# Kernel tuning notes

Hardware: AMD Instinct MI355X
Metric: run time of the kernel (lower is better)

The kernel has to match this reference:

```python
import jax, jax.numpy as jnp
import numpy as np

N1 = 100000  # source cloud size (x1)
N2 = 100000  # target cloud size (x2)
F = 64       # point feature dim
E = 1600000  # number of radius edges (avg 16 neighbors)
H = 128      # MLP hidden/out dim


def setup_inputs() -> dict:
    key = jax.random.key(0)
    ks = jax.random.split(key, 12)
    s = 0.05
    return {
        "x1_features": jax.random.normal(ks[0], (N1, F), jnp.float32),
        "x1_pos": jax.random.normal(ks[1], (N1, 3), jnp.float32),
        "x2_features": jax.random.normal(ks[2], (N2, F), jnp.float32),
        "x2_pos": jax.random.normal(ks[3], (N2, 3), jnp.float32),
        "W1": jax.random.normal(ks[4], (2 * F + 3, H), jnp.float32) * s,
        "b1": jnp.zeros((H,), jnp.float32),
        "W2": jax.random.normal(ks[5], (H, H), jnp.float32) * s,
        "b2": jnp.zeros((H,), jnp.float32),
        "W3": jax.random.normal(ks[6], (H, H), jnp.float32) * s,
        "b3": jnp.zeros((H,), jnp.float32),
        "edge_src": jax.random.randint(ks[7], (E,), 0, N1, jnp.int32),
        "edge_dst": jax.random.randint(ks[8], (E,), 0, N2, jnp.int32),
    }


def reference(x1_features, x1_pos, x2_features, x2_pos,
              W1, b1, W2, b2, W3, b3, edge_src, edge_dst):
    # message(x_i, x_j, pos_i, pos_j): i = target (x2, edge_dst), j = source (x1, edge_src)
    # msg = cat([x_i, x_j, pos_j - pos_i], dim=1)  -> [E, 2F+3]
    msg = jnp.concatenate(
        [x2_features[edge_dst],
         x1_features[edge_src],
         x1_pos[edge_src] - x2_pos[edge_dst]], axis=1)
    # MLP (Linear+ReLU x3, FastFlow3D make_mlp style)
    h = jax.nn.relu(msg @ W1 + b1)
    h = jax.nn.relu(h @ W2 + b2)
    h = jax.nn.relu(h @ W3 + b3)
    # scatter-max aggregation onto x2 nodes; PyG fills empty segments with 0
    out = jax.ops.segment_max(h, edge_dst, num_segments=N2)
    out = jnp.where(jnp.isneginf(out), 0.0, out)
    return out, x2_pos
```

## Files before the change

### kernel.cpp

```cpp
#include <hip/hip_runtime.h>
#include <hip/hip_bf16.h>

#define DEV __device__ __forceinline__

typedef short bf16x8 __attribute__((ext_vector_type(8)));
typedef float f32x16 __attribute__((ext_vector_type(16)));
typedef unsigned short u16x2 __attribute__((ext_vector_type(2)));

static constexpr int FDIM = 64;
static constexpr int HH   = 128;
static constexpr int TM   = 512;
static constexpr int CH   = 4096;
static constexpr int NCH  = 27;
static constexpr int WB   = NCH * CH;
static constexpr int WT_ELEMS = NCH * 2048;

DEV unsigned pack2(float a, float b) {
    union { __hip_bfloat162 h; unsigned u; } cv;
    cv.h.x = __float2bfloat16(a);
    cv.h.y = __float2bfloat16(b);
    return cv.u;
}
DEV unsigned short f2bf(float f) {
    union { __hip_bfloat16 h; unsigned short u; } cv;
    cv.h = __float2bfloat16(f);
    return cv.u;
}
DEV unsigned pmax2(unsigned a, unsigned b) {
    u16x2 av = __builtin_bit_cast(u16x2, a);
    u16x2 bv = __builtin_bit_cast(u16x2, b);
    return __builtin_bit_cast(unsigned, __builtin_elementwise_max(av, bv));
}

__global__ void k_cvt(const float* __restrict__ src, unsigned short* __restrict__ dst, int n8) {
    int i = blockIdx.x * 256 + threadIdx.x;
    if (i < n8) {
        float4 a = *(const float4*)(src + (size_t)i * 8);
        float4 b = *(const float4*)(src + (size_t)i * 8 + 4);
        uint4 o;
        o.x = pack2(a.x, a.y); o.y = pack2(a.z, a.w);
        o.z = pack2(b.x, b.y); o.w = pack2(b.z, b.w);
        *(uint4*)(dst + (size_t)i * 8) = o;
    }
}

__global__ void k_wprep(const float* __restrict__ W1, const float* __restrict__ b1,
                        const float* __restrict__ W2, const float* __restrict__ b2,
                        const float* __restrict__ W3, const float* __restrict__ b3,
                        unsigned short* __restrict__ wt) {
    int i = blockIdx.x * 256 + threadIdx.x;
    if (i >= WT_ELEMS) return;
    int c = i >> 11, r = i & 2047;
    int n = r >> 4, half = (r >> 3) & 1, e = r & 7;
    int layer = c / 9, ks = c % 9;
    int k = ks * 16 + half * 8 + e;
    float v = 0.f;
    if (layer == 0) {
        if (k < 131) v = W1[k * HH + n];
        else if (k == 131) v = b1[n];
    } else {
        const float* W = (layer == 1) ? W2 : W3;
        const float* b = (layer == 1) ? b2 : b3;
        if (k < 128) v = W[k * HH + n];
        else if (k == 128) v = b[n];
    }
    wt[i] = f2bf(v);
}

__global__ void k_hist(const int* __restrict__ edst, int* __restrict__ cnt, int E) {
    int e = blockIdx.x * 256 + threadIdx.x;
    if (e < E) atomicAdd(&cnt[edst[e]], 1);
}

__global__ void k_scan_part(const int* __restrict__ cnt, int* __restrict__ partial, int n2) {
    __shared__ int sm[256];
    int t = threadIdx.x;
    int base = blockIdx.x * 1024 + t * 4;
    int s = 0;
#pragma unroll
    for (int j = 0; j < 4; j++) { int idx = base + j; if (idx < n2) s += cnt[idx]; }
    sm[t] = s; __syncthreads();
    for (int off = 128; off > 0; off >>= 1) {
        if (t < off) sm[t] += sm[t + off];
        __syncthreads();
    }
    if (t == 0) partial[blockIdx.x] = sm[0];
}

__global__ void k_scan_top(int* __restrict__ partial, int nb) {
    __shared__ int sm[256];
    int t = threadIdx.x;
    int v = (t < nb) ? partial[t] : 0;
    sm[t] = v; __syncthreads();
    for (int off = 1; off < 256; off <<= 1) {
        int add = (t >= off) ? sm[t - off] : 0;
        __syncthreads();
        sm[t] += add;
        __syncthreads();
    }
    if (t < nb) partial[t] = sm[t] - v;
}

__global__ void k_scan_down(const int* __restrict__ cnt, const int* __restrict__ partial,
                            int* __restrict__ cursor, int n2) {
    __shared__ int sm[256];
    int t = threadIdx.x;
    int base = blockIdx.x * 1024 + t * 4;
    int c[4]; int s = 0;
#pragma unroll
    for (int j = 0; j < 4; j++) { int idx = base + j; c[j] = (idx < n2) ? cnt[idx] : 0; s += c[j]; }
    sm[t] = s; __syncthreads();
    for (int off = 1; off < 256; off <<= 1) {
        int add = (t >= off) ? sm[t - off] : 0;
        __syncthreads();
        sm[t] += add;
        __syncthreads();
    }
    int run = partial[blockIdx.x] + (sm[t] - s);
#pragma unroll
    for (int j = 0; j < 4; j++) {
        int idx = base + j;
        if (idx < n2) cursor[idx] = run;
        run += c[j];
    }
}

__global__ void k_fill(const int* __restrict__ edst, const int* __restrict__ esrc,
                       int* __restrict__ cursor,
                       int* __restrict__ csr_s, int* __restrict__ csr_d, int E) {
    int e = blockIdx.x * 256 + threadIdx.x;
    if (e < E) {
        int d = edst[e];
        int p = atomicAdd(&cursor[d], 1);
        csr_s[p] = esrc[e];
        csr_d[p] = d;
    }
}

DEV f32x16 zerov() {
    f32x16 v;
#pragma unroll
    for (int i = 0; i < 16; i++) v[i] = 0.f;
    return v;
}
DEV float relu(float x) { return fmaxf(x, 0.f); }

DEV void layer_reg(const char* __restrict__ wl, const unsigned pkin[32],
                   unsigned pkout[32], int l31, int hh, unsigned biasw) {
    unsigned xv[16];
#pragma unroll
    for (int ks = 0; ks < 8; ks++) {
        unsigned t0 = hh ? pkin[4 * ks + 0] : pkin[4 * ks + 2];
        unsigned t1 = hh ? pkin[4 * ks + 1] : pkin[4 * ks + 3];
        xv[2 * ks + 0] = (unsigned)__shfl_xor((int)t0, 32, 64);
        xv[2 * ks + 1] = (unsigned)__shfl_xor((int)t1, 32, 64);
    }
#pragma unroll
    for (int rt = 0; rt < 4; rt++) {
        const char* arow = wl + (rt * 32 + l31) * 32 + hh * 16;
        f32x16 acc = zerov();
#pragma unroll
        for (int ks = 0; ks < 8; ks++) {
            union { unsigned u[4]; bf16x8 v; } B;
            B.u[0] = hh ? xv[2 * ks + 0]   : pkin[4 * ks + 0];
            B.u[1] = hh ? xv[2 * ks + 1]   : pkin[4 * ks + 1];
            B.u[2] = hh ? pkin[4 * ks + 2] : xv[2 * ks + 0];
            B.u[3] = hh ? pkin[4 * ks + 3] : xv[2 * ks + 1];
            bf16x8 A = *(const bf16x8*)(arow + ks * CH);
            acc = __builtin_amdgcn_mfma_f32_32x32x16_bf16(A, B.v, acc, 0, 0, 0);
        }
        {
            union { unsigned u[4]; bf16x8 v; } B;
            B.u[0] = biasw; B.u[1] = 0u; B.u[2] = 0u; B.u[3] = 0u;
            bf16x8 A = *(const bf16x8*)(arow + 8 * CH);
            acc = __builtin_amdgcn_mfma_f32_32x32x16_bf16(A, B.v, acc, 0, 0, 0);
        }
#pragma unroll
        for (int g = 0; g < 4; g++) {
            pkout[8 * rt + 2 * g + 0] = pack2(relu(acc[4 * g + 0]), relu(acc[4 * g + 1]));
            pkout[8 * rt + 2 * g + 1] = pack2(relu(acc[4 * g + 2]), relu(acc[4 * g + 3]));
        }
    }
}

template <bool SORTED, bool BF16SRC>
__global__ __launch_bounds__(1024, 4) void k_main(
    const float* __restrict__ x1f, const float* __restrict__ x1p,
    const float* __restrict__ x2f, const float* __restrict__ x2p,
    const char* __restrict__ xb1, const char* __restrict__ xb2,
    const unsigned short* __restrict__ wt,
    const int* __restrict__ csr_s, const int* __restrict__ csr_d,
    const int* __restrict__ edge_src, const int* __restrict__ edge_dst,
    float* __restrict__ out, int E) {
    __shared__ __align__(16) char wlds[WB];

    const int tid  = threadIdx.x;
    const int lane = tid & 63;
    const int wv   = tid >> 6;
    const int l31  = lane & 31;
    const int hh   = lane >> 5;
    const int eb   = blockIdx.x * TM;

    {
        const uint4* src = (const uint4*)wt;
        uint4* dst = (uint4*)wlds;
#pragma unroll
        for (int j = tid; j < WB / 16; j += 1024)
            dst[j] = src[j];
    }
    __syncthreads();

    const int r    = wv * 32 + l31;
    const int slot = eb + r;
    const bool ok  = slot < E;
    int d = -1, s = 0;
    if (ok) {
        d = SORTED ? csr_d[slot] : edge_dst[slot];
        s = SORTED ? csr_s[slot] : edge_src[slot];
    }
    const int dg = (d < 0) ? 0 : d;
    const int sg = s;

    bf16x8 Bv[9];
    if (BF16SRC) {
        const char* bx2 = xb2 + (size_t)dg * (2 * FDIM);
        const char* bx1 = xb1 + (size_t)sg * (2 * FDIM);
#pragma unroll
        for (int ks = 0; ks < 4; ks++)
            Bv[ks] = *(const bf16x8*)(bx2 + (2 * ks + hh) * 16);
#pragma unroll
        for (int ks = 4; ks < 8; ks++)
            Bv[ks] = *(const bf16x8*)(bx1 + (2 * (ks - 4) + hh) * 16);
    } else {
        const float* fx2 = x2f + (size_t)dg * FDIM;
        const float* fx1 = x1f + (size_t)sg * FDIM;
#pragma unroll
        for (int ks = 0; ks < 8; ks++) {
            const float* b = (ks < 4) ? (fx2 + (2 * ks + hh) * 8)
                                      : (fx1 + (2 * (ks - 4) + hh) * 8);
            float4 a0 = *(const float4*)(b);
            float4 a1 = *(const float4*)(b + 4);
            union { unsigned u[4]; bf16x8 v; } B;
            B.u[0] = pack2(a0.x, a0.y); B.u[1] = pack2(a0.z, a0.w);
            B.u[2] = pack2(a1.x, a1.y); B.u[3] = pack2(a1.z, a1.w);
            Bv[ks] = B.v;
        }
    }
    {
        float dx = 0.f, dy = 0.f, dz = 0.f;
        if (ok) {
            dx = x1p[sg * 3 + 0] - x2p[dg * 3 + 0];
            dy = x1p[sg * 3 + 1] - x2p[dg * 3 + 1];
            dz = x1p[sg * 3 + 2] - x2p[dg * 3 + 2];
        }
        union { unsigned u[4]; bf16x8 v; } P;
        P.u[0] = hh ? 0u : pack2(dx, dy);
        P.u[1] = hh ? 0u : pack2(dz, 1.0f);
        P.u[2] = 0u; P.u[3] = 0u;
        Bv[8] = P.v;
    }

    unsigned pkA[32], pkB[32];
#pragma unroll
    for (int rt = 0; rt < 4; rt++) {
        const char* arow = wlds + (rt * 32 + l31) * 32 + hh * 16;
        f32x16 acc = zerov();
#pragma unroll
        for (int ks = 0; ks < 9; ks++) {
            bf16x8 A = *(const bf16x8*)(arow + ks * CH);
            acc = __builtin_amdgcn_mfma_f32_32x32x16_bf16(A, Bv[ks], acc, 0, 0, 0);
        }
#pragma unroll
        for (int g = 0; g < 4; g++) {
            pkA[8 * rt + 2 * g + 0] = pack2(relu(acc[4 * g + 0]), relu(acc[4 * g + 1]));
            pkA[8 * rt + 2 * g + 1] = pack2(relu(acc[4 * g + 2]), relu(acc[4 * g + 3]));
        }
    }

    const unsigned biasw = hh ? 0u : 0x00003F80u;
    layer_reg(wlds + 9 * CH,  pkA, pkB, l31, hh, biasw);
    layer_reg(wlds + 18 * CH, pkB, pkA, l31, hh, biasw);

    const int dn = __shfl_down(d, 1, 32);
#pragma unroll
    for (int off = 1; off < 32; off <<= 1) {
        int nd = __shfl_up(d, off, 32);
        bool take = (l31 >= off) && (nd == d);
#pragma unroll
        for (int u = 0; u < 32; u++) {
            unsigned nv = (unsigned)__shfl_up((int)pkA[u], off, 32);
            unsigned mx = pmax2(pkA[u], nv);
            pkA[u] = take ? mx : pkA[u];
        }
    }
    const bool flush = (d >= 0) && ((l31 == 31) || (dn != d));
    if (flush) {
        int* op = (int*)out + (size_t)d * HH;
#pragma unroll
        for (int u = 0; u < 32; u++) {
            const int feat = 32 * (u >> 3) + 8 * ((u >> 1) & 3) + 4 * hh + 2 * (u & 1);
            unsigned w = pkA[u];
            float lo = __uint_as_float(w << 16);
            float hi = __uint_as_float(w & 0xffff0000u);
            if (lo > 0.f) atomicMax(op + feat,     __float_as_int(lo));
            if (hi > 0.f) atomicMax(op + feat + 1, __float_as_int(hi));
        }
    }
}

extern "C" void kernel_launch(void* const* d_in, const int* in_sizes, int n_in,
                              void* d_out, int out_size, void* d_ws, size_t ws_size,
                              hipStream_t stream) {
    const float* x1f = (const float*)d_in[0];
    const float* x1p = (const float*)d_in[1];
    const float* x2f = (const float*)d_in[2];
    const float* x2p = (const float*)d_in[3];
    const float* W1  = (const float*)d_in[4];
    const float* b1  = (const float*)d_in[5];
    const float* W2  = (const float*)d_in[6];
    const float* b2  = (const float*)d_in[7];
    const float* W3  = (const float*)d_in[8];
    const float* b3  = (const float*)d_in[9];
    const int* esrc  = (const int*)d_in[10];
    const int* edst  = (const int*)d_in[11];
    const int E  = in_sizes[10];
    const int N1 = in_sizes[1] / 3;
    const int N2 = in_sizes[3] / 3;
    float* out = (float*)d_out;

    size_t off = 0;
    auto take = [&](size_t bytes) { size_t o = off; off = (off + bytes + 255) & ~(size_t)255; return o; };
    size_t o_cnt = take(4 * (size_t)N2);
    size_t o_cur = take(4 * (size_t)N2);
    size_t o_par = take(4 * 256);
    size_t o_cs  = take(4 * (size_t)E);
    size_t o_cd  = take(4 * (size_t)E);
    size_t o_wt  = take(2 * (size_t)WT_ELEMS);
    size_t need_csr = off;
    size_t o_x1  = take(2 * (size_t)N1 * FDIM);
    size_t o_x2  = take(2 * (size_t)N2 * FDIM);
    size_t need_bf = off;

    const int NB = (N2 + 1023) / 1024;
    bool use_csr = (need_csr <= ws_size) && (NB <= 256);
    bool use_bf  = (need_bf <= ws_size);

    char* ws = (char*)d_ws;
    unsigned short* wt = use_csr ? (unsigned short*)(ws + o_wt) : (unsigned short*)ws;
    int* cnt    = (int*)(ws + o_cnt);
    int* cursor = (int*)(ws + o_cur);
    int* part   = (int*)(ws + o_par);
    int* csr_s  = (int*)(ws + o_cs);
    int* csr_d  = (int*)(ws + o_cd);
    char* xb1   = ws + o_x1;
    char* xb2   = ws + o_x2;

    (void)hipMemsetAsync(out, 0, (size_t)N2 * HH * 4, stream);
    (void)hipMemcpyAsync(out + (size_t)N2 * HH, x2p, (size_t)N2 * 3 * 4,
                         hipMemcpyDeviceToDevice, stream);

    k_wprep<<<(WT_ELEMS + 255) / 256, 256, 0, stream>>>(W1, b1, W2, b2, W3, b3, wt);

    if (use_bf) {
        int n8_1 = N1 * FDIM / 8, n8_2 = N2 * FDIM / 8;
        k_cvt<<<(n8_1 + 255) / 256, 256, 0, stream>>>(x1f, (unsigned short*)xb1, n8_1);
        k_cvt<<<(n8_2 + 255) / 256, 256, 0, stream>>>(x2f, (unsigned short*)xb2, n8_2);
    }

    const int grid = (E + TM - 1) / TM;
    if (use_csr) {
        (void)hipMemsetAsync(cnt, 0, 4 * (size_t)N2, stream);
        k_hist<<<(E + 255) / 256, 256, 0, stream>>>(edst, cnt, E);
        k_scan_part<<<NB, 256, 0, stream>>>(cnt, part, N2);
        k_scan_top<<<1, 256, 0, stream>>>(part, NB);
        k_scan_down<<<NB, 256, 0, stream>>>(cnt, part, cursor, N2);
        k_fill<<<(E + 255) / 256, 256, 0, stream>>>(edst, esrc, cursor, csr_s, csr_d, E);
        if (use_bf)
            k_main<true, true><<<grid, 1024, 0, stream>>>(
                x1f, x1p, x2f, x2p, xb1, xb2, wt, csr_s, csr_d, esrc, edst, out, E);
        else
            k_main<true, false><<<grid, 1024, 0, stream>>>(
                x1f, x1p, x2f, x2p, xb1, xb2, wt, csr_s, csr_d, esrc, edst, out, E);
    } else {
        if (use_bf)
            k_main<false, true><<<grid, 1024, 0, stream>>>(
                x1f, x1p, x2f, x2p, xb1, xb2, wt, edst, edst, esrc, edst, out, E);
        else
            k_main<false, false><<<grid, 1024, 0, stream>>>(
                x1f, x1p, x2f, x2p, xb1, xb2, wt, edst, edst, esrc, edst, out, E);
    }
}
```

Before: 664.7 us.

## Read MLP weights from global, shrink blocks, DPP segment scan, direct stores for interior segments

Stops staging all 108KB of weights into LDS per block and has the MFMA operands read straight from global/L2, with 256-thread blocks of 128 edges. The per-block LDS fill, the barrier and the LDS occupancy limit go away, at the cost of repeated global weight loads. The segmented max scan now uses DPP row moves instead of shuffles. The CSR src/dst arrays are packed into one int2 array. Destinations whose whole segment sits inside one 32-lane group write with plain float4 stores instead of atomics.

Result: slower. 693.8 us (+4.4%).

```diff
diff --git a/kernel.cpp b/kernel.cpp
--- a/kernel.cpp
+++ b/kernel.cpp
@@ -9,10 +9,9 @@
 
 static constexpr int FDIM = 64;
 static constexpr int HH   = 128;
-static constexpr int TM   = 512;
+static constexpr int TM   = 128;
 static constexpr int CH   = 4096;
 static constexpr int NCH  = 27;
-static constexpr int WB   = NCH * CH;
 static constexpr int WT_ELEMS = NCH * 2048;
 
 DEV unsigned pack2(float a, float b) {
@@ -30,6 +29,10 @@
     u16x2 av = __builtin_bit_cast(u16x2, a);
     u16x2 bv = __builtin_bit_cast(u16x2, b);
     return __builtin_bit_cast(unsigned, __builtin_elementwise_max(av, bv));
+}
+template <int CTRL>
+DEV int dppmov(int x) {
+    return __builtin_amdgcn_update_dpp(x, x, CTRL, 0xf, 0xf, false);
 }
 
 __global__ void k_cvt(const float* __restrict__ src, unsigned short* __restrict__ dst, int n8) {
@@ -126,14 +129,12 @@
 }
 
 __global__ void k_fill(const int* __restrict__ edst, const int* __restrict__ esrc,
-                       int* __restrict__ cursor,
-                       int* __restrict__ csr_s, int* __restrict__ csr_d, int E) {
+                       int* __restrict__ cursor, int2* __restrict__ csr_sd, int E) {
     int e = blockIdx.x * 256 + threadIdx.x;
     if (e < E) {
         int d = edst[e];
         int p = atomicAdd(&cursor[d], 1);
-        csr_s[p] = esrc[e];
-        csr_d[p] = d;
+        csr_sd[p] = make_int2(esrc[e], d);
     }
 }
 
@@ -184,39 +185,27 @@
 }
 
 template <bool SORTED, bool BF16SRC>
-__global__ __launch_bounds__(1024, 4) void k_main(
+__global__ __launch_bounds__(256, 6) void k_main(
     const float* __restrict__ x1f, const float* __restrict__ x1p,
     const float* __restrict__ x2f, const float* __restrict__ x2p,
     const char* __restrict__ xb1, const char* __restrict__ xb2,
-    const unsigned short* __restrict__ wt,
-    const int* __restrict__ csr_s, const int* __restrict__ csr_d,
+    const char* __restrict__ wt,
+    const int2* __restrict__ csr_sd,
     const int* __restrict__ edge_src, const int* __restrict__ edge_dst,
     float* __restrict__ out, int E) {
-    __shared__ __align__(16) char wlds[WB];
-
     const int tid  = threadIdx.x;
     const int lane = tid & 63;
     const int wv   = tid >> 6;
     const int l31  = lane & 31;
     const int hh   = lane >> 5;
-    const int eb   = blockIdx.x * TM;
-
-    {
-        const uint4* src = (const uint4*)wt;
-        uint4* dst = (uint4*)wlds;
-#pragma unroll
-        for (int j = tid; j < WB / 16; j += 1024)
-            dst[j] = src[j];
-    }
-    __syncthreads();
-
     const int r    = wv * 32 + l31;
-    const int slot = eb + r;
+    const int slot = blockIdx.x * TM + r;
     const bool ok  = slot < E;
+
     int d = -1, s = 0;
     if (ok) {
-        d = SORTED ? csr_d[slot] : edge_dst[slot];
-        s = SORTED ? csr_s[slot] : edge_src[slot];
+        if (SORTED) { int2 sd = csr_sd[slot]; s = sd.x; d = sd.y; }
+        else        { d = edge_dst[slot]; s = edge_src[slot]; }
     }
     const int dg = (d < 0) ? 0 : d;
     const int sg = s;
@@ -263,7 +252,7 @@
     unsigned pkA[32], pkB[32];
 #pragma unroll
     for (int rt = 0; rt < 4; rt++) {
-        const char* arow = wlds + (rt * 32 + l31) * 32 + hh * 16;
+        const char* arow = wt + (rt * 32 + l31) * 32 + hh * 16;
         f32x16 acc = zerov();
 #pragma unroll
         for (int ks = 0; ks < 9; ks++) {
@@ -278,32 +267,59 @@
     }
 
     const unsigned biasw = hh ? 0u : 0x00003F80u;
-    layer_reg(wlds + 9 * CH,  pkA, pkB, l31, hh, biasw);
-    layer_reg(wlds + 18 * CH, pkB, pkA, l31, hh, biasw);
+    layer_reg(wt + 9 * CH,  pkA, pkB, l31, hh, biasw);
+    layer_reg(wt + 18 * CH, pkB, pkA, l31, hh, biasw);
+
+#define SCAN_STEP(CTRL, EXTRA)                                            \
+    {                                                                     \
+        int dsft = dppmov<CTRL>(d);                                       \
+        bool take = (dsft == d) EXTRA;                                    \
+        _Pragma("unroll")                                                 \
+        for (int u = 0; u < 32; u++) {                                    \
+            int sv = dppmov<CTRL>((int)pkA[u]);                           \
+            unsigned mx = pmax2(pkA[u], (unsigned)sv);                    \
+            pkA[u] = take ? mx : pkA[u];                                  \
+        }                                                                 \
+    }
+    SCAN_STEP(0x111, )
+    SCAN_STEP(0x112, )
+    SCAN_STEP(0x114, )
+    SCAN_STEP(0x118, )
+    SCAN_STEP(0x142, && (l31 >= 16))
+#undef SCAN_STEP
 
     const int dn = __shfl_down(d, 1, 32);
-#pragma unroll
-    for (int off = 1; off < 32; off <<= 1) {
-        int nd = __shfl_up(d, off, 32);
-        bool take = (l31 >= off) && (nd == d);
-#pragma unroll
-        for (int u = 0; u < 32; u++) {
-            unsigned nv = (unsigned)__shfl_up((int)pkA[u], off, 32);
-            unsigned mx = pmax2(pkA[u], nv);
-            pkA[u] = take ? mx : pkA[u];
-        }
-    }
-    const bool flush = (d >= 0) && ((l31 == 31) || (dn != d));
-    if (flush) {
-        int* op = (int*)out + (size_t)d * HH;
-#pragma unroll
-        for (int u = 0; u < 32; u++) {
-            const int feat = 32 * (u >> 3) + 8 * ((u >> 1) & 3) + 4 * hh + 2 * (u & 1);
-            unsigned w = pkA[u];
-            float lo = __uint_as_float(w << 16);
-            float hi = __uint_as_float(w & 0xffff0000u);
-            if (lo > 0.f) atomicMax(op + feat,     __float_as_int(lo));
-            if (hi > 0.f) atomicMax(op + feat + 1, __float_as_int(hi));
+    const int dp = __shfl_up(d, 1, 32);
+    unsigned long long startm = __ballot(dp != d) | 0x0000000100000001ull;
+    const bool isflush = (d >= 0) && ((l31 == 31) || (dn != d));
+    if (isflush) {
+        unsigned long long below = startm & (~0ull >> (63 - lane));
+        int sbit = 63 - __builtin_clzll(below);
+        bool interior = ((sbit & 31) != 0) && (l31 != 31);
+        float* orow = out + (size_t)d * HH;
+        if (interior) {
+#pragma unroll
+            for (int g = 0; g < 16; g++) {
+                const int F = 32 * (g >> 2) + 8 * (g & 3) + 4 * hh;
+                unsigned w0 = pkA[2 * g], w1 = pkA[2 * g + 1];
+                float4 v;
+                v.x = __uint_as_float(w0 << 16);
+                v.y = __uint_as_float(w0 & 0xffff0000u);
+                v.z = __uint_as_float(w1 << 16);
+                v.w = __uint_as_float(w1 & 0xffff0000u);
+                *(float4*)(orow + F) = v;
+            }
+        } else {
+            int* op = (int*)orow;
+#pragma unroll
+            for (int u = 0; u < 32; u++) {
+                const int feat = 32 * (u >> 3) + 8 * ((u >> 1) & 3) + 4 * hh + 2 * (u & 1);
+                unsigned w = pkA[u];
+                float lo = __uint_as_float(w << 16);
+                float hi = __uint_as_float(w & 0xffff0000u);
+                if (lo > 0.f) atomicMax(op + feat,     __float_as_int(lo));
+                if (hi > 0.f) atomicMax(op + feat + 1, __float_as_int(hi));
+            }
         }
     }
 }
@@ -333,8 +349,7 @@
     size_t o_cnt = take(4 * (size_t)N2);
     size_t o_cur = take(4 * (size_t)N2);
     size_t o_par = take(4 * 256);
-    size_t o_cs  = take(4 * (size_t)E);
-    size_t o_cd  = take(4 * (size_t)E);
+    size_t o_csd = take(8 * (size_t)E);
     size_t o_wt  = take(2 * (size_t)WT_ELEMS);
     size_t need_csr = off;
     size_t o_x1  = take(2 * (size_t)N1 * FDIM);
@@ -347,13 +362,12 @@
 
     char* ws = (char*)d_ws;
     unsigned short* wt = use_csr ? (unsigned short*)(ws + o_wt) : (unsigned short*)ws;
-    int* cnt    = (int*)(ws + o_cnt);
-    int* cursor = (int*)(ws + o_cur);
-    int* part   = (int*)(ws + o_par);
-    int* csr_s  = (int*)(ws + o_cs);
-    int* csr_d  = (int*)(ws + o_cd);
-    char* xb1   = ws + o_x1;
-    char* xb2   = ws + o_x2;
+    int*  cnt    = (int*)(ws + o_cnt);
+    int*  cursor = (int*)(ws + o_cur);
+    int*  part   = (int*)(ws + o_par);
+    int2* csr_sd = (int2*)(ws + o_csd);
+    char* xb1    = ws + o_x1;
+    char* xb2    = ws + o_x2;
 
     (void)hipMemsetAsync(out, 0, (size_t)N2 * HH * 4, stream);
     (void)hipMemcpyAsync(out + (size_t)N2 * HH, x2p, (size_t)N2 * 3 * 4,
@@ -374,19 +388,19 @@
         k_scan_part<<<NB, 256, 0, stream>>>(cnt, part, N2);
         k_scan_top<<<1, 256, 0, stream>>>(part, NB);
         k_scan_down<<<NB, 256, 0, stream>>>(cnt, part, cursor, N2);
-        k_fill<<<(E + 255) / 256, 256, 0, stream>>>(edst, esrc, cursor, csr_s, csr_d, E);
+        k_fill<<<(E + 255) / 256, 256, 0, stream>>>(edst, esrc, cursor, csr_sd, E);
         if (use_bf)
-            k_main<true, true><<<grid, 1024, 0, stream>>>(
-                x1f, x1p, x2f, x2p, xb1, xb2, wt, csr_s, csr_d, esrc, edst, out, E);
+            k_main<true, true><<<grid, 256, 0, stream>>>(
+                x1f, x1p, x2f, x2p, xb1, xb2, (const char*)wt, csr_sd, esrc, edst, out, E);
         else
-            k_main<true, false><<<grid, 1024, 0, stream>>>(
-                x1f, x1p, x2f, x2p, xb1, xb2, wt, csr_s, csr_d, esrc, edst, out, E);
+            k_main<true, false><<<grid, 256, 0, stream>>>(
+                x1f, x1p, x2f, x2p, xb1, xb2, (const char*)wt, csr_sd, esrc, edst, out, E);
     } else {
         if (use_bf)
-            k_main<false, true><<<grid, 1024, 0, stream>>>(
-                x1f, x1p, x2f, x2p, xb1, xb2, wt, edst, edst, esrc, edst, out, E);
+            k_main<false, true><<<grid, 256, 0, stream>>>(
+                x1f, x1p, x2f, x2p, xb1, xb2, (const char*)wt, csr_sd, esrc, edst, out, E);
         else
-            k_main<false, false><<<grid, 1024, 0, stream>>>(
-                x1f, x1p, x2f, x2p, xb1, xb2, wt, edst, edst, esrc, edst, out, E);
-    }
-}
+            k_main<false, false><<<grid, 256, 0, stream>>>(
+                x1f, x1p, x2f, x2p, xb1, xb2, (const char*)wt, csr_sd, esrc, edst, out, E);
+    }
+}
```
